# Optimization experiments

Measured on AMD Instinct MI355X. Metric: run time of the kernel, lower is better.

## Reference

```python
import jax, jax.numpy as jnp
import numpy as np

B, C, N = 2, 512, 2048
HEADS, DIM_HEAD, SCALE = 16, 64, 8.0
H_DIM = HEADS * DIM_HEAD
EPS = 1e-12  # F.normalize default eps


def setup_inputs() -> dict:
    key = jax.random.key(0)
    ks = jax.random.split(key, 5)
    x = jax.random.normal(ks[0], (B, C, N), dtype=jnp.float32)
    Wqkv = jax.random.normal(ks[1], (3 * H_DIM, C), dtype=jnp.float32) * (1.0 / np.sqrt(C))
    q_scale = jnp.ones((DIM_HEAD,), dtype=jnp.float32)
    k_scale = jnp.ones((DIM_HEAD,), dtype=jnp.float32)
    Wout = jax.random.normal(ks[2], (C, H_DIM), dtype=jnp.float32) * (1.0 / np.sqrt(H_DIM))
    bout = jax.random.normal(ks[3], (C,), dtype=jnp.float32) * 0.01
    return {"x": x, "Wqkv": Wqkv, "q_scale": q_scale, "k_scale": k_scale,
            "Wout": Wout, "bout": bout}


def _l2norm(t):
    # F.normalize(t, dim=-1): t / max(||t||, eps)
    n = jnp.sqrt(jnp.sum(t * t, axis=-1, keepdims=True))
    return t / jnp.maximum(n, EPS)


def reference(x, Wqkv, q_scale, k_scale, Wout, bout):
    # 1x1 conv == pointwise matmul over channel dim
    qkv = jnp.einsum('oc,bcn->bon', Wqkv, x)              # [B, 3*H_DIM, N]
    q, k, v = jnp.split(qkv, 3, axis=1)
    # unflatten channels -> [B, H, D, N]
    def to_heads(t):
        return t.reshape(B, HEADS, DIM_HEAD, N)
    q, k, v = map(to_heads, (q, k, v))
    # cosine attention: l2-normalize q,k over head dim, apply learned per-dim scales
    q = _l2norm(q.transpose(0, 1, 3, 2)) * q_scale        # [B, H, N, D]
    k = _l2norm(k.transpose(0, 1, 3, 2)) * k_scale        # [B, H, N, D]
    sim = jnp.einsum('bhid,bhjd->bhij', q, k) * SCALE     # [B, H, N, N]
    attn = jax.nn.softmax(sim, axis=-1)
    out = jnp.einsum('bhij,bhdj->bhid', attn, v)          # [B, H, N, D]
    out = out.transpose(0, 1, 3, 2).reshape(B, H_DIM, N)  # b h n d -> b (h d) n
    return jnp.einsum('oc,bcn->bon', Wout, out) + bout[None, :, None]
```

## Files before the change

### kernel.cpp

```cpp
#include <hip/hip_runtime.h>
#include <hip/hip_bf16.h>

#define BATCH 2
#define CCH   512
#define NSEQ  2048
#define HEADS 16
#define DHEAD 64
#define HDIM  1024
#define ODIM  3072
#define QK_PRESCALE 11.541560327111707f

typedef short short4v __attribute__((ext_vector_type(4)));
typedef short short8 __attribute__((ext_vector_type(8)));
typedef float float4v __attribute__((ext_vector_type(4)));
typedef int   int4v   __attribute__((ext_vector_type(4)));

__device__ __forceinline__ unsigned short f2bf(float f) {
    unsigned int u = __float_as_uint(f);
    return (unsigned short)((u + 0x7FFFu + ((u >> 16) & 1u)) >> 16);
}
__device__ __forceinline__ unsigned short f2bf_fast(float f) {
    return (unsigned short)((__float_as_uint(f) + 0x8000u) >> 16);
}
__device__ __forceinline__ float fexp2(float x) {
#if __has_builtin(__builtin_amdgcn_exp2f)
    return __builtin_amdgcn_exp2f(x);
#else
    return exp2f(x);
#endif
}
__device__ __forceinline__ int pack_bf16(float lo, float hi) {
#if __has_builtin(__builtin_amdgcn_cvt_pk_bf16_f32)
    typedef __bf16 bf2_t __attribute__((ext_vector_type(2)));
    bf2_t v = __builtin_amdgcn_cvt_pk_bf16_f32(lo, hi);
    return __builtin_bit_cast(int, v);
#else
    return (int)f2bf_fast(lo) | ((int)(unsigned)f2bf_fast(hi) << 16);
#endif
}

typedef __attribute__((address_space(1))) const void* as1_cvp;
typedef __attribute__((address_space(3))) void* as3_vp;
__device__ __forceinline__ void cp16(const void* g, void* l) {
    __builtin_amdgcn_global_load_lds((as1_cvp)g, (as3_vp)l, 16, 0, 0);
}
__global__ __launch_bounds__(256) void k_prep(
    const float* __restrict__ Wqkv, const float* __restrict__ Wout,
    const float* __restrict__ x,
    const float* __restrict__ qs, const float* __restrict__ ks,
    unsigned short* __restrict__ Wqkvb, unsigned short* __restrict__ Woutb,
    unsigned short* __restrict__ xt, float* __restrict__ M) {
    const int bx = blockIdx.x;
    if (bx < 2048) {
        if (bx == 0 && threadIdx.x < 64) {
            int lane = threadIdx.x;
            float p = fabsf(qs[lane] * ks[lane]);
#pragma unroll
            for (int off = 1; off < 64; off <<= 1) p = fmaxf(p, __shfl_xor(p, off));
            if (lane == 0) *M = QK_PRESCALE * p;
        }
        int i4 = (bx * 256 + threadIdx.x) * 4;
        const float* src; unsigned short* dst; int idx;
        if (i4 < ODIM * CCH) { src = Wqkv; dst = Wqkvb; idx = i4; }
        else { src = Wout; dst = Woutb; idx = i4 - ODIM * CCH; }
        float4 v = *(const float4*)(src + idx);
        ushort4 o;
        o.x = f2bf(v.x); o.y = f2bf(v.y); o.z = f2bf(v.z); o.w = f2bf(v.w);
        *(ushort4*)(dst + idx) = o;
        return;
    }
    __shared__ unsigned short t[64][65];
    const int fx = bx - 2048;
    const int n0 = (fx & 31) * 64;
    const int c0 = ((fx >> 5) & 7) * 64;
    const int b  = fx >> 8;
    const int tr = threadIdx.x >> 6, tc = threadIdx.x & 63;
    const float* xs = x + (size_t)b * CCH * NSEQ;
    unsigned short* xd = xt + (size_t)b * NSEQ * CCH;
#pragma unroll
    for (int r = 0; r < 16; ++r) {
        int c = r * 4 + tr;
        t[c][tc] = f2bf(xs[(size_t)(c0 + c) * NSEQ + n0 + tc]);
    }
    __syncthreads();
#pragma unroll
    for (int r = 0; r < 16; ++r) {
        int n = r * 4 + tr;
        xd[(size_t)(n0 + n) * CCH + c0 + tc] = t[tc][n];
    }
}

__global__ __launch_bounds__(256) void k_gemm_qkv(
    const unsigned short* __restrict__ W, const unsigned short* __restrict__ xt,
    const float* __restrict__ qs, const float* __restrict__ ks,
    unsigned short* __restrict__ qh, unsigned short* __restrict__ kh,
    unsigned short* __restrict__ vb) {
    constexpr int K = CCH, N = NSEQ;
    __shared__ __align__(16) short smem[2 * 128 * 64];
    short* lsA = smem;
    short* lsB = smem + 128 * 64;
    const int tid = threadIdx.x, wave = tid >> 6, lane = tid & 63;
    const int l15 = lane & 15, quad = lane >> 4;
    const int n0 = blockIdx.x * 128, m0 = blockIdx.y * 128, z = blockIdx.z;
    const short* Ab = (const short*)W + (size_t)m0 * K;
    const short* Bb = (const short*)xt + ((size_t)z * N + n0) * K;
    const int wm = wave >> 1, wn = wave & 1;
    const int cswz = (((tid & 7) ^ ((tid >> 3) & 7))) * 8;
    const int sw7 = (l15 & 7);

    float4v acc[4][4];
#pragma unroll
    for (int i = 0; i < 4; ++i)
#pragma unroll
        for (int j = 0; j < 4; ++j) acc[i][j] = (float4v){0.f, 0.f, 0.f, 0.f};

    for (int k0 = 0; k0 < K; k0 += 64) {
#pragma unroll
        for (int it = 0; it < 4; ++it) {
            int row = it * 32 + (tid >> 3);
            cp16(Ab + (size_t)row * K + k0 + cswz, &lsA[it * 2048 + wave * 512]);
            cp16(Bb + (size_t)row * K + k0 + cswz, &lsB[it * 2048 + wave * 512]);
        }
        __syncthreads();
        short8 af[4][2], bfr[4][2];
#pragma unroll
        for (int t = 0; t < 4; ++t)
#pragma unroll
            for (int kk = 0; kk < 2; ++kk) {
                af[t][kk]  = *(const short8*)&lsA[(wm * 64 + t * 16 + l15) * 64 + ((kk * 4 + quad) ^ sw7) * 8];
                bfr[t][kk] = *(const short8*)&lsB[(wn * 64 + t * 16 + l15) * 64 + ((kk * 4 + quad) ^ sw7) * 8];
            }
#pragma unroll
        for (int mt = 0; mt < 4; ++mt)
#pragma unroll
            for (int nt = 0; nt < 4; ++nt) {
                acc[mt][nt] = __builtin_amdgcn_mfma_f32_16x16x32_bf16(af[mt][0], bfr[nt][0], acc[mt][nt], 0, 0, 0);
                acc[mt][nt] = __builtin_amdgcn_mfma_f32_16x16x32_bf16(af[mt][1], bfr[nt][1], acc[mt][nt], 0, 0, 0);
            }
        __syncthreads();
    }

    const int co   = (m0 + wm * 64) >> 6;
    const int part = co >> 4;
    const int h    = co & 15;
    const int bh   = z * HEADS + h;
    short* myT = smem + wave * 4096;

    if (part < 2) {
        float inv[4];
#pragma unroll
        for (int nt = 0; nt < 4; ++nt) {
            float ss = 0.f;
#pragma unroll
            for (int mt = 0; mt < 4; ++mt)
#pragma unroll
                for (int r = 0; r < 4; ++r) ss += acc[mt][nt][r] * acc[mt][nt][r];
            ss += __shfl_xor(ss, 16);
            ss += __shfl_xor(ss, 32);
            inv[nt] = 1.0f / fmaxf(sqrtf(ss), 1e-12f);
        }
        const float* sc = part ? ks : qs;
        const float csc = part ? 1.0f : QK_PRESCALE;
#pragma unroll
        for (int mt = 0; mt < 4; ++mt) {
            const int db = mt * 16 + quad * 4;
            float4 s4 = *(const float4*)(sc + db);
            s4.x *= csc; s4.y *= csc; s4.z *= csc; s4.w *= csc;
#pragma unroll
            for (int nt = 0; nt < 4; ++nt) {
                int nl = nt * 16 + l15;
                short4v o;
                o.x = (short)f2bf(acc[mt][nt][0] * inv[nt] * s4.x);
                o.y = (short)f2bf(acc[mt][nt][1] * inv[nt] * s4.y);
                o.z = (short)f2bf(acc[mt][nt][2] * inv[nt] * s4.z);
                o.w = (short)f2bf(acc[mt][nt][3] * inv[nt] * s4.w);
                *(short4v*)&myT[nl * 64 + (((db >> 3) ^ (nl & 7)) << 3) + (db & 7)] = o;
            }
        }
        unsigned short* dst = (part ? kh : qh) + (size_t)bh * NSEQ * DHEAD
                              + (size_t)(n0 + wn * 64) * DHEAD;
#pragma unroll
        for (int pass = 0; pass < 8; ++pass) {
            int nl = pass * 8 + (lane >> 3), c = lane & 7;
            short8 vv = *(const short8*)&myT[nl * 64 + ((c ^ (nl & 7)) << 3)];
            *(short8*)&dst[(size_t)nl * DHEAD + c * 8] = vv;
        }
    } else {
#pragma unroll
        for (int mt = 0; mt < 4; ++mt)
#pragma unroll
            for (int nt = 0; nt < 4; ++nt) {
                int nl = nt * 16 + l15;
                int swc = nl >> 3, swo = nl & 7;
#pragma unroll
                for (int r = 0; r < 4; ++r) {
                    int d = mt * 16 + quad * 4 + r;
                    myT[d * 64 + ((swc ^ (d & 7)) << 3) + swo] = (short)f2bf(acc[mt][nt][r]);
                }
            }
        unsigned short* dst = vb + (size_t)bh * DHEAD * NSEQ + n0 + wn * 64;
#pragma unroll
        for (int pass = 0; pass < 8; ++pass) {
            int d = pass * 8 + (lane >> 3), c = lane & 7;
            short8 vv = *(const short8*)&myT[d * 64 + ((c ^ (d & 7)) << 3)];
            *(short8*)&dst[(size_t)d * NSEQ + c * 8] = vv;
        }
    }
}

__global__ __launch_bounds__(256, 2) void k_attn(
    const unsigned short* __restrict__ qh, const unsigned short* __restrict__ kh,
    const unsigned short* __restrict__ vb,
    unsigned short* __restrict__ aot, const float* __restrict__ Mptr) {
    __shared__ __align__(16) short Kt[2][64 * 64];
    __shared__ __align__(16) short Vt[2][64 * 64];
    const int tid = threadIdx.x, wave = tid >> 6, lane = tid & 63;
    const int l15 = lane & 15, quad = lane >> 4, q8 = quad * 8;
    const int flat = blockIdx.x;
    const int xcd = flat & 7, idx = flat >> 3;
    const int bh = xcd * 4 + (idx >> 4);
    const int i0 = (idx & 15) * 128;
    const int b = bh >> 4, h = bh & 15;
    const float Ms = *Mptr;
    const float4v mInit = (float4v){-Ms, -Ms, -Ms, -Ms};
    const int srow = tid >> 3;
    const int kkey  = (srow & 3) | (((srow >> 3) & 1) << 2);
    const int cswzK = ((tid & 7) ^ kkey) * 8;
    const int cswzV = ((tid & 7) ^ (srow & 7)) * 8;
    const int ksw = l15 & 7;
    const int kc0 = ((0 + quad) ^ ksw) * 8;
    const int kc1 = ((4 + quad) ^ ksw) * 8;
    const int ar0 = (l15 >> 2) * 8 + (l15 & 3);
    const int ar1 = ar0 + 4;

    short8 qf[2][2];
    {
        const short* qb = (const short*)qh + ((size_t)bh * NSEQ + i0 + wave * 32) * DHEAD;
#pragma unroll
        for (int it = 0; it < 2; ++it) {
            qf[it][0] = *(const short8*)&qb[(it * 16 + l15) * DHEAD + q8];
            qf[it][1] = *(const short8*)&qb[(it * 16 + l15) * DHEAD + 32 + q8];
        }
    }

    float4v of[2][4];
#pragma unroll
    for (int it = 0; it < 2; ++it)
#pragma unroll
        for (int dt = 0; dt < 4; ++dt) of[it][dt] = (float4v){0.f, 0.f, 0.f, 0.f};
    float l_acc[2] = {0.f, 0.f};

    const short* kbase = (const short*)kh + (size_t)bh * NSEQ * DHEAD;
    const short* vbase = (const short*)vb + (size_t)bh * DHEAD * NSEQ;

#pragma unroll
    for (int it = 0; it < 2; ++it) {
        int row = it * 32 + srow;
        cp16(kbase + (size_t)row * DHEAD + cswzK, &Kt[0][it * 2048 + wave * 512]);
        cp16(vbase + (size_t)row * NSEQ + cswzV, &Vt[0][it * 2048 + wave * 512]);
    }
    __syncthreads();

    int buf = 0;
    for (int j0 = 0; j0 < NSEQ; j0 += 64) {
        if (j0 + 64 < NSEQ) {
            int nb = buf ^ 1;
#pragma unroll
            for (int it = 0; it < 2; ++it) {
                int row = it * 32 + srow;
                cp16(kbase + (size_t)(j0 + 64 + row) * DHEAD + cswzK, &Kt[nb][it * 2048 + wave * 512]);
                cp16(vbase + (size_t)row * NSEQ + j0 + 64 + cswzV, &Vt[nb][it * 2048 + wave * 512]);
            }
        }

#pragma unroll
        for (int ch = 0; ch < 2; ++ch) {
            short8 av[4];
#pragma unroll
            for (int dt = 0; dt < 4; ++dt) {
                int vrow = dt * 16 + l15;
                av[dt] = *(const short8*)&Vt[buf][vrow * 64 + (((ch * 4 + quad) ^ (l15 & 7))) * 8];
            }
            int4v pw[2];
#pragma unroll
            for (int t = 0; t < 2; ++t) {
                const int arow = ch * 32 + (t ? ar1 : ar0);
                const short* kr = &Kt[buf][arow * 64];
                short8 kf0 = *(const short8*)&kr[kc0];
                short8 kf1 = *(const short8*)&kr[kc1];
#pragma unroll
                for (int it = 0; it < 2; ++it) {
                    float4v s = mInit;
                    s = __builtin_amdgcn_mfma_f32_16x16x32_bf16(kf0, qf[it][0], s, 0, 0, 0);
                    s = __builtin_amdgcn_mfma_f32_16x16x32_bf16(kf1, qf[it][1], s, 0, 0, 0);
                    float p0 = fexp2(s[0]);
                    float p1 = fexp2(s[1]);
                    float p2 = fexp2(s[2]);
                    float p3 = fexp2(s[3]);
                    l_acc[it] += (p0 + p1) + (p2 + p3);
                    pw[it][t * 2 + 0] = pack_bf16(p0, p1);
                    pw[it][t * 2 + 1] = pack_bf16(p2, p3);
                }
            }
            short8 pb0 = __builtin_bit_cast(short8, pw[0]);
            short8 pb1 = __builtin_bit_cast(short8, pw[1]);
#pragma unroll
            for (int dt = 0; dt < 4; ++dt) {
                of[0][dt] = __builtin_amdgcn_mfma_f32_16x16x32_bf16(av[dt], pb0, of[0][dt], 0, 0, 0);
                of[1][dt] = __builtin_amdgcn_mfma_f32_16x16x32_bf16(av[dt], pb1, of[1][dt], 0, 0, 0);
            }
        }

        __syncthreads();
        buf ^= 1;
    }

#pragma unroll
    for (int it = 0; it < 2; ++it) {
        float l = l_acc[it];
        l += __shfl_xor(l, 16);
        l += __shfl_xor(l, 32);
        float inv = 1.0f / fmaxf(l, 1e-30f);
        unsigned short* ob = aot + ((size_t)b * NSEQ + i0 + wave * 32 + it * 16 + l15) * HDIM + h * DHEAD;
#pragma unroll
        for (int dt = 0; dt < 4; ++dt) {
            ushort4 o;
            o.x = f2bf(of[it][dt][0] * inv);
            o.y = f2bf(of[it][dt][1] * inv);
            o.z = f2bf(of[it][dt][2] * inv);
            o.w = f2bf(of[it][dt][3] * inv);
            *(ushort4*)&ob[dt * 16 + quad * 4] = o;
        }
    }
}

__global__ __launch_bounds__(256) void k_gemm_out(
    const unsigned short* __restrict__ W, const unsigned short* __restrict__ aot,
    const float* __restrict__ bias, float* __restrict__ out) {
    constexpr int K = HDIM, N = NSEQ, M = CCH;
    __shared__ __align__(16) short lsA[64 * 64];
    __shared__ __align__(16) short lsB[64 * 64];
    const int tid = threadIdx.x, wave = tid >> 6, lane = tid & 63;
    const int l15 = lane & 15, quad = lane >> 4;
    const int n0 = blockIdx.x * 64, m0 = blockIdx.y * 64, z = blockIdx.z;
    const short* Ab = (const short*)W + (size_t)m0 * K;
    const short* Bb = (const short*)aot + ((size_t)z * N + n0) * K;
    const int wm = wave >> 1, wn = wave & 1;
    const int cswz = (((tid & 7) ^ ((tid >> 3) & 7))) * 8;
    const int sw7 = (l15 & 7);

    float4v acc[2][2];
#pragma unroll
    for (int i = 0; i < 2; ++i)
#pragma unroll
        for (int j = 0; j < 2; ++j) acc[i][j] = (float4v){0.f, 0.f, 0.f, 0.f};

    for (int k0 = 0; k0 < K; k0 += 64) {
        {
            int row = tid >> 3;
            cp16(Ab + (size_t)row * K + k0 + cswz, &lsA[wave * 512]);
            cp16(Ab + (size_t)(row + 32) * K + k0 + cswz, &lsA[2048 + wave * 512]);
            cp16(Bb + (size_t)row * K + k0 + cswz, &lsB[wave * 512]);
            cp16(Bb + (size_t)(row + 32) * K + k0 + cswz, &lsB[2048 + wave * 512]);
        }
        __syncthreads();
        short8 af[2][2], bfr[2][2];
#pragma unroll
        for (int t = 0; t < 2; ++t)
#pragma unroll
            for (int kk = 0; kk < 2; ++kk) {
                af[t][kk]  = *(const short8*)&lsA[(wm * 32 + t * 16 + l15) * 64 + ((kk * 4 + quad) ^ sw7) * 8];
                bfr[t][kk] = *(const short8*)&lsB[(wn * 32 + t * 16 + l15) * 64 + ((kk * 4 + quad) ^ sw7) * 8];
            }
#pragma unroll
        for (int mt = 0; mt < 2; ++mt)
#pragma unroll
            for (int nt = 0; nt < 2; ++nt) {
                acc[mt][nt] = __builtin_amdgcn_mfma_f32_16x16x32_bf16(af[mt][0], bfr[nt][0], acc[mt][nt], 0, 0, 0);
                acc[mt][nt] = __builtin_amdgcn_mfma_f32_16x16x32_bf16(af[mt][1], bfr[nt][1], acc[mt][nt], 0, 0, 0);
            }
        __syncthreads();
    }
    float* Co = out + (size_t)z * M * N;
#pragma unroll
    for (int mt = 0; mt < 2; ++mt)
#pragma unroll
        for (int nt = 0; nt < 2; ++nt) {
            int mrow = m0 + wm * 32 + mt * 16 + quad * 4;
#pragma unroll
            for (int r = 0; r < 4; ++r) {
                int mr = mrow + r;
                int nc = n0 + wn * 32 + nt * 16 + l15;
                Co[(size_t)mr * N + nc] = acc[mt][nt][r] + bias[mr];
            }
        }
}

extern "C" void kernel_launch(void* const* d_in, const int* in_sizes, int n_in,
                              void* d_out, int out_size, void* d_ws, size_t ws_size,
                              hipStream_t stream) {
    const float* x = nullptr; const float* Wqkv = nullptr;
    const float* qs = nullptr; const float* ks = nullptr;
    const float* Wout = nullptr; const float* bout = nullptr;
    for (int i = 0; i < n_in; ++i) {
        switch (in_sizes[i]) {
            case BATCH * CCH * NSEQ: x    = (const float*)d_in[i]; break;
            case ODIM * CCH:         Wqkv = (const float*)d_in[i]; break;
            case CCH * HDIM:         Wout = (const float*)d_in[i]; break;
            case CCH:                bout = (const float*)d_in[i]; break;
            case DHEAD: if (!qs) qs = (const float*)d_in[i]; else ks = (const float*)d_in[i]; break;
            default: break;
        }
    }
    float* y = (float*)d_out;

    char* ws = (char*)d_ws;
    float*          Mbuf  = (float*)(ws + 0);
    unsigned short* Wqkvb = (unsigned short*)(ws + 4096);
    unsigned short* Woutb = (unsigned short*)(ws + 3149824);
    unsigned short* xt    = (unsigned short*)(ws + 4198400);
    unsigned short* qh    = (unsigned short*)(ws + 8392704);
    unsigned short* kh    = (unsigned short*)(ws + 16781312);
    unsigned short* vb    = (unsigned short*)(ws + 25169920);
    unsigned short* aot   = (unsigned short*)(ws + 33558528);

    k_prep<<<dim3(2048 + 512), 256, 0, stream>>>(Wqkv, Wout, x, qs, ks, Wqkvb, Woutb, xt, Mbuf);
    k_gemm_qkv<<<dim3(NSEQ / 128, ODIM / 128, BATCH), 256, 0, stream>>>(Wqkvb, xt, qs, ks, qh, kh, vb);
    k_attn<<<dim3(512), 256, 0, stream>>>(qh, kh, vb, aot, Mbuf);
    k_gemm_out<<<dim3(NSEQ / 64, CCH / 64, BATCH), 256, 0, stream>>>(Woutb, aot, bout, y);
}
```

Before: 147.1 us.

## Split attention key range across two wave groups per block with LDS reduction

The attention kernel now launches 512 threads per block. Two groups of four waves each process half of the key/value sequence for the same 128 queries, using separate double-buffered LDS tiles. Group 1 writes its partial outputs and row sums to LDS, and group 0 adds them, normalizes and stores. This doubles the waves per query tile so more latency can be hidden with the same grid of 512 blocks. The cost is a larger LDS footprint, a reduction step at the end, and possibly lower occupancy under the new launch bounds.

Result: no change. 150.0 us (+1.9%).

```diff
diff --git a/kernel.cpp b/kernel.cpp
--- a/kernel.cpp
+++ b/kernel.cpp
@@ -208,13 +208,15 @@
     }
 }
 
-__global__ __launch_bounds__(256, 2) void k_attn(
+__global__ __launch_bounds__(512, 4) void k_attn(
     const unsigned short* __restrict__ qh, const unsigned short* __restrict__ kh,
     const unsigned short* __restrict__ vb,
     unsigned short* __restrict__ aot, const float* __restrict__ Mptr) {
-    __shared__ __align__(16) short Kt[2][64 * 64];
-    __shared__ __align__(16) short Vt[2][64 * 64];
+    __shared__ __align__(16) short Kt[2][2][64 * 64];
+    __shared__ __align__(16) short Vt[2][2][64 * 64];
     const int tid = threadIdx.x, wave = tid >> 6, lane = tid & 63;
+    const int grp = wave >> 2, w4 = wave & 3;
+    const int gtid = tid & 255;
     const int l15 = lane & 15, quad = lane >> 4, q8 = quad * 8;
     const int flat = blockIdx.x;
     const int xcd = flat & 7, idx = flat >> 3;
@@ -223,19 +225,20 @@
     const int b = bh >> 4, h = bh & 15;
     const float Ms = *Mptr;
     const float4v mInit = (float4v){-Ms, -Ms, -Ms, -Ms};
-    const int srow = tid >> 3;
+    const int srow = gtid >> 3;
     const int kkey  = (srow & 3) | (((srow >> 3) & 1) << 2);
-    const int cswzK = ((tid & 7) ^ kkey) * 8;
-    const int cswzV = ((tid & 7) ^ (srow & 7)) * 8;
+    const int cswzK = ((gtid & 7) ^ kkey) * 8;
+    const int cswzV = ((gtid & 7) ^ (srow & 7)) * 8;
     const int ksw = l15 & 7;
     const int kc0 = ((0 + quad) ^ ksw) * 8;
     const int kc1 = ((4 + quad) ^ ksw) * 8;
     const int ar0 = (l15 >> 2) * 8 + (l15 & 3);
     const int ar1 = ar0 + 4;
+    const int jbase = grp * (NSEQ / 2);
 
     short8 qf[2][2];
     {
-        const short* qb = (const short*)qh + ((size_t)bh * NSEQ + i0 + wave * 32) * DHEAD;
+        const short* qb = (const short*)qh + ((size_t)bh * NSEQ + i0 + w4 * 32) * DHEAD;
 #pragma unroll
         for (int it = 0; it < 2; ++it) {
             qf[it][0] = *(const short8*)&qb[(it * 16 + l15) * DHEAD + q8];
@@ -250,26 +253,26 @@
         for (int dt = 0; dt < 4; ++dt) of[it][dt] = (float4v){0.f, 0.f, 0.f, 0.f};
     float l_acc[2] = {0.f, 0.f};
 
-    const short* kbase = (const short*)kh + (size_t)bh * NSEQ * DHEAD;
-    const short* vbase = (const short*)vb + (size_t)bh * DHEAD * NSEQ;
+    const short* kbase = (const short*)kh + ((size_t)bh * NSEQ + jbase) * DHEAD;
+    const short* vbase = (const short*)vb + (size_t)bh * DHEAD * NSEQ + jbase;
 
 #pragma unroll
     for (int it = 0; it < 2; ++it) {
         int row = it * 32 + srow;
-        cp16(kbase + (size_t)row * DHEAD + cswzK, &Kt[0][it * 2048 + wave * 512]);
-        cp16(vbase + (size_t)row * NSEQ + cswzV, &Vt[0][it * 2048 + wave * 512]);
+        cp16(kbase + (size_t)row * DHEAD + cswzK, &Kt[grp][0][it * 2048 + w4 * 512]);
+        cp16(vbase + (size_t)row * NSEQ + cswzV, &Vt[grp][0][it * 2048 + w4 * 512]);
     }
     __syncthreads();
 
     int buf = 0;
-    for (int j0 = 0; j0 < NSEQ; j0 += 64) {
-        if (j0 + 64 < NSEQ) {
+    for (int j0 = 0; j0 < NSEQ / 2; j0 += 64) {
+        if (j0 + 64 < NSEQ / 2) {
             int nb = buf ^ 1;
 #pragma unroll
             for (int it = 0; it < 2; ++it) {
                 int row = it * 32 + srow;
-                cp16(kbase + (size_t)(j0 + 64 + row) * DHEAD + cswzK, &Kt[nb][it * 2048 + wave * 512]);
-                cp16(vbase + (size_t)row * NSEQ + j0 + 64 + cswzV, &Vt[nb][it * 2048 + wave * 512]);
+                cp16(kbase + (size_t)(j0 + 64 + row) * DHEAD + cswzK, &Kt[grp][nb][it * 2048 + w4 * 512]);
+                cp16(vbase + (size_t)row * NSEQ + j0 + 64 + cswzV, &Vt[grp][nb][it * 2048 + w4 * 512]);
             }
         }
 
@@ -279,13 +282,13 @@
 #pragma unroll
             for (int dt = 0; dt < 4; ++dt) {
                 int vrow = dt * 16 + l15;
-                av[dt] = *(const short8*)&Vt[buf][vrow * 64 + (((ch * 4 + quad) ^ (l15 & 7))) * 8];
+                av[dt] = *(const short8*)&Vt[grp][buf][vrow * 64 + (((ch * 4 + quad) ^ (l15 & 7))) * 8];
             }
             int4v pw[2];
 #pragma unroll
             for (int t = 0; t < 2; ++t) {
                 const int arow = ch * 32 + (t ? ar1 : ar0);
-                const short* kr = &Kt[buf][arow * 64];
+                const short* kr = &Kt[grp][buf][arow * 64];
                 short8 kf0 = *(const short8*)&kr[kc0];
                 short8 kf1 = *(const short8*)&kr[kc1];
 #pragma unroll
@@ -315,21 +318,43 @@
         buf ^= 1;
     }
 
+    float lred[2];
 #pragma unroll
     for (int it = 0; it < 2; ++it) {
         float l = l_acc[it];
         l += __shfl_xor(l, 16);
         l += __shfl_xor(l, 32);
-        float inv = 1.0f / fmaxf(l, 1e-30f);
-        unsigned short* ob = aot + ((size_t)b * NSEQ + i0 + wave * 32 + it * 16 + l15) * HDIM + h * DHEAD;
-#pragma unroll
-        for (int dt = 0; dt < 4; ++dt) {
-            ushort4 o;
-            o.x = f2bf(of[it][dt][0] * inv);
-            o.y = f2bf(of[it][dt][1] * inv);
-            o.z = f2bf(of[it][dt][2] * inv);
-            o.w = f2bf(of[it][dt][3] * inv);
-            *(ushort4*)&ob[dt * 16 + quad * 4] = o;
+        lred[it] = l;
+    }
+
+    float* F = (float*)&Kt[0][0][0];
+    float* L = (float*)&Vt[0][0][0];
+    if (grp == 1) {
+#pragma unroll
+        for (int it = 0; it < 2; ++it) {
+#pragma unroll
+            for (int dt = 0; dt < 4; ++dt)
+                *(float4v*)&F[(((w4 * 2 + it) * 4 + dt) * 64 + lane) * 4] = of[it][dt];
+            L[(w4 * 2 + it) * 64 + lane] = lred[it];
+        }
+    }
+    __syncthreads();
+    if (grp == 0) {
+#pragma unroll
+        for (int it = 0; it < 2; ++it) {
+            float lt = lred[it] + L[(w4 * 2 + it) * 64 + lane];
+            float inv = 1.0f / fmaxf(lt, 1e-30f);
+            unsigned short* ob = aot + ((size_t)b * NSEQ + i0 + w4 * 32 + it * 16 + l15) * HDIM + h * DHEAD;
+#pragma unroll
+            for (int dt = 0; dt < 4; ++dt) {
+                float4v p = *(const float4v*)&F[(((w4 * 2 + it) * 4 + dt) * 64 + lane) * 4];
+                ushort4 o;
+                o.x = f2bf((of[it][dt][0] + p[0]) * inv);
+                o.y = f2bf((of[it][dt][1] + p[1]) * inv);
+                o.z = f2bf((of[it][dt][2] + p[2]) * inv);
+                o.w = f2bf((of[it][dt][3] + p[3]) * inv);
+                *(ushort4*)&ob[dt * 16 + quad * 4] = o;
+            }
         }
     }
 }
@@ -426,6 +451,6 @@
 
     k_prep<<<dim3(2048 + 512), 256, 0, stream>>>(Wqkv, Wout, x, qs, ks, Wqkvb, Woutb, xt, Mbuf);
     k_gemm_qkv<<<dim3(NSEQ / 128, ODIM / 128, BATCH), 256, 0, stream>>>(Wqkvb, xt, qs, ks, qh, kh, vb);
-    k_attn<<<dim3(512), 256, 0, stream>>>(qh, kh, vb, aot, Mbuf);
+    k_attn<<<dim3(512), 512, 0, stream>>>(qh, kh, vb, aot, Mbuf);
     k_gemm_out<<<dim3(NSEQ / 64, CCH / 64, BATCH), 256, 0, stream>>>(Woutb, aot, bout, y);
 }
```
